# Optimization experiments

Measured on AMD Instinct MI355X. Metric: run time of the kernel, lower is better.

Reference implementation:

```python
import jax, jax.numpy as jnp
import numpy as np

EPS = 1e-09

def setup_inputs() -> dict:
    key = jax.random.key(0)
    k1, k2 = jax.random.split(key)
    N, D = 8192, 1024
    src_pos = jax.random.normal(k1, (N, D), dtype=jnp.float32)
    trg_pos = jax.random.normal(k2, (N, D), dtype=jnp.float32)
    return {"src_pos": src_pos, "trg_pos": trg_pos, "batch_size": N}

def reference(src_pos, trg_pos, batch_size):
    # [N, N] pairwise similarity (computed once; original redundantly does it twice)
    S = jnp.einsum('nd,md->nm', src_pos, trg_pos)
    S_xi_yi = jnp.diagonal(S)                      # [N] positive-pair scores
    lse = jax.nn.logsumexp(S, axis=1)              # [N] stable log-sum-exp over rows
    n = src_pos.shape[0]                           # matches torch assert fallback
    return -((S_xi_yi - lse).sum() / n) + EPS
```

## Files before the change

### kernel.cpp

```cpp
#include <hip/hip_runtime.h>
#include <hip/hip_bf16.h>
#include <math.h>

typedef __attribute__((ext_vector_type(4))) int   i32x4;
typedef __attribute__((ext_vector_type(4))) float f32x4;

#define NTOT 8192
#define DIM  1024
#define NCHUNK 128
#define QSCALE 20.0f
#define INV_S2 (1.0f / (QSCALE * QSCALE))

__device__ __forceinline__ void gload_lds16(const void* g, void* l) {
  __builtin_amdgcn_global_load_lds(
      (const __attribute__((address_space(1))) unsigned int*)g,
      (__attribute__((address_space(3))) unsigned int*)l,
      16, 0, 0);
}

#define SBAR() do { __builtin_amdgcn_sched_barrier(0); __builtin_amdgcn_s_barrier(); } while (0)

#define MFMA_PH(MQ, NQ, A, B)                                                        \
  do {                                                                               \
    __builtin_amdgcn_s_setprio(1);                                                   \
    _Pragma("unroll")                                                                \
    for (int fm = 0; fm < 4; ++fm) {                                                 \
      _Pragma("unroll")                                                              \
      for (int fn = 0; fn < 2; ++fn) {                                               \
        acc[(MQ)*4+fm][(NQ)*2+fn] = __builtin_amdgcn_mfma_i32_16x16x64_i8(           \
            A[fm][0], B[fn][0], acc[(MQ)*4+fm][(NQ)*2+fn], 0, 0, 0);                 \
        acc[(MQ)*4+fm][(NQ)*2+fn] = __builtin_amdgcn_mfma_i32_16x16x64_i8(           \
            A[fm][1], B[fn][1], acc[(MQ)*4+fm][(NQ)*2+fn], 0, 0, 0);                 \
      }                                                                              \
    }                                                                                \
    __builtin_amdgcn_s_setprio(0);                                                   \
  } while (0)

__global__ __launch_bounds__(256)
void convert_diag(const float* __restrict__ src, const float* __restrict__ trg,
                  unsigned int* __restrict__ A8, unsigned int* __restrict__ B8,
                  float* __restrict__ diag) {
  const int row  = blockIdx.x * 4 + (threadIdx.x >> 6);
  const int lane = threadIdx.x & 63;
  const f32x4* a = (const f32x4*)(src + (size_t)row * DIM);
  const f32x4* b = (const f32x4*)(trg + (size_t)row * DIM);
  float s = 0.f;
#pragma unroll
  for (int j = 0; j < 4; ++j) {
    f32x4 x = a[j * 64 + lane];
    f32x4 y = b[j * 64 + lane];
    s += x.x * y.x + x.y * y.y + x.z * y.z + x.w * y.w;
    unsigned pa = 0, pb = 0;
#pragma unroll
    for (int e = 0; e < 4; ++e) {
      float xf = (e == 0) ? x.x : (e == 1) ? x.y : (e == 2) ? x.z : x.w;
      float yf = (e == 0) ? y.x : (e == 1) ? y.y : (e == 2) ? y.z : y.w;
      int qa = (int)rintf(fminf(fmaxf(xf * QSCALE, -127.f), 127.f));
      int qb = (int)rintf(fminf(fmaxf(yf * QSCALE, -127.f), 127.f));
      pa |= ((unsigned)qa & 0xFFu) << (8 * e);
      pb |= ((unsigned)qb & 0xFFu) << (8 * e);
    }
    A8[(size_t)row * 256 + j * 64 + lane] = pa;
    B8[(size_t)row * 256 + j * 64 + lane] = pb;
  }
#pragma unroll
  for (int off = 32; off; off >>= 1) s += __shfl_xor(s, off);
  if (lane == 0) diag[row] = s;
}

__global__ __launch_bounds__(512, 2)
void gemm_lse(const unsigned char* __restrict__ A8, const unsigned char* __restrict__ B8,
              float2* __restrict__ partials) {
  __shared__ __align__(16) char lds[131072];
  char* As = lds;
  char* Bs = lds + 65536;

  const int tid  = threadIdx.x;
  const int lane = tid & 63;
  const int wid  = tid >> 6;
  const int wr = wid >> 2, wc = wid & 3;
  const int bx = blockIdx.x, by = blockIdx.y;
  const int row0 = by * 256, col0 = bx * 256;

  const int lrow = tid >> 3;
  const int lchk = tid & 7;
  const int schk = lchk ^ (lrow & 7);

  auto stageA = [&](int b, int h, int t) {
#pragma unroll
    for (int hi = 0; hi < 2; ++hi) {
      char* dst = As + (((b * 2 + h) * 2 + hi) << 13) + lrow * 128 + lchk * 16;
      const unsigned char* srcp = A8 + (size_t)(row0 + hi * 128 + h * 64 + lrow) * DIM
                                     + t * 128 + schk * 16;
      gload_lds16(srcp, dst);
    }
  };
  auto stageB = [&](int b, int h, int t) {
#pragma unroll
    for (int j = 0; j < 2; ++j) {
      char* dst = Bs + ((b * 2 + h) << 14) + j * 8192 + lrow * 128 + lchk * 16;
      const unsigned char* srcp = B8 + (size_t)(col0 + (2 * j + (lrow >> 5)) * 64 + h * 32 + (lrow & 31)) * DIM
                                     + t * 128 + schk * 16;
      gload_lds16(srcp, dst);
    }
  };

  const int arow = (lane & 15) * 128;
  const int kb0 = (((lane >> 4) * 16)     ) ^ ((lane & 7) << 4);
  const int kb1 = (((lane >> 4) * 16) + 64) ^ ((lane & 7) << 4);

  auto rdA = [&](i32x4 (&a)[4][2], int b, int h) {
    const char* base = As + (((b * 2 + h) * 2 + wr) << 13);
#pragma unroll
    for (int f = 0; f < 4; ++f) {
      a[f][0] = *(const i32x4*)(base + f * 2048 + arow + kb0);
      a[f][1] = *(const i32x4*)(base + f * 2048 + arow + kb1);
    }
  };
  auto rdB = [&](i32x4 (&bb)[2][2], int b, int h) {
    const char* base = Bs + ((b * 2 + h) << 14) + wc * 4096;
#pragma unroll
    for (int f = 0; f < 2; ++f) {
      bb[f][0] = *(const i32x4*)(base + f * 2048 + arow + kb0);
      bb[f][1] = *(const i32x4*)(base + f * 2048 + arow + kb1);
    }
  };

  i32x4 acc[8][4] = {};
  i32x4 a_lo[4][2], a_hi[4][2], b_lo[2][2], b_hi[2][2];

  stageA(0, 0, 0); stageA(0, 1, 0); stageB(0, 0, 0); stageB(0, 1, 0);
  stageA(1, 0, 1); stageB(1, 0, 1); stageB(1, 1, 1);
  asm volatile("s_waitcnt vmcnt(6)" ::: "memory");
  SBAR();

  for (int i = 0; i < 4; ++i) {
    const bool last = (i == 3);
    const int t1 = 2 * i + 1, t2 = 2 * i + 2, t3 = 2 * i + 3;

    rdA(a_lo, 0, 0); rdB(b_lo, 0, 0);
    stageA(1, 1, t1);
    SBAR();
    MFMA_PH(0, 0, a_lo, b_lo);
    SBAR();

    rdB(b_hi, 0, 1);
    if (!last) stageA(0, 0, t2);
    SBAR();
    MFMA_PH(0, 1, a_lo, b_hi);
    SBAR();

    rdA(a_hi, 0, 1);
    if (!last) stageB(0, 0, t2);
    SBAR();
    MFMA_PH(1, 1, a_hi, b_hi);
    SBAR();

    if (!last) stageB(0, 1, t2);
    SBAR();
    MFMA_PH(1, 0, a_hi, b_lo);
    if (last) { asm volatile("s_waitcnt vmcnt(0)" ::: "memory"); }
    else      { asm volatile("s_waitcnt vmcnt(6)" ::: "memory"); }
    SBAR();

    rdA(a_lo, 1, 0); rdB(b_lo, 1, 0);
    if (!last) stageA(0, 1, t2);
    SBAR();
    MFMA_PH(0, 0, a_lo, b_lo);
    SBAR();

    rdB(b_hi, 1, 1);
    if (!last) stageA(1, 0, t3);
    SBAR();
    MFMA_PH(0, 1, a_lo, b_hi);
    SBAR();

    rdA(a_hi, 1, 1);
    if (!last) stageB(1, 0, t3);
    SBAR();
    MFMA_PH(1, 1, a_hi, b_hi);
    SBAR();

    if (!last) stageB(1, 1, t3);
    SBAR();
    MFMA_PH(1, 0, a_hi, b_lo);
    if (!last) { asm volatile("s_waitcnt vmcnt(6)" ::: "memory"); }
    SBAR();
  }

  const int rbase  = row0 + wr * 128 + ((lane >> 4) << 2);
  const int cchunk = bx * 4 + wc;
#pragma unroll
  for (int mi = 0; mi < 8; ++mi) {
#pragma unroll
    for (int j = 0; j < 4; ++j) {
      int im = max(max(acc[mi][0][j], acc[mi][1][j]),
                   max(acc[mi][2][j], acc[mi][3][j]));
#pragma unroll
      for (int off = 8; off; off >>= 1) im = max(im, __shfl_xor(im, off));
      float l = 0.f;
#pragma unroll
      for (int ni = 0; ni < 4; ++ni)
        l += __expf((float)(acc[mi][ni][j] - im) * INV_S2);
#pragma unroll
      for (int off = 8; off; off >>= 1) l += __shfl_xor(l, off);
      if ((lane & 15) == 0)
        partials[(size_t)(rbase + mi * 16 + j) * NCHUNK + cchunk] =
            make_float2((float)im * INV_S2, l);
    }
  }
}

__global__ __launch_bounds__(256)
void row_lse_kernel(const float2* __restrict__ partials,
                    const float* __restrict__ diag,
                    float* __restrict__ rowval) {
  const int row  = (blockIdx.x * 256 + threadIdx.x) >> 6;
  const int lane = threadIdx.x & 63;
  if (row >= NTOT) return;
  const float2 p0 = partials[(size_t)row * NCHUNK + lane];
  const float2 p1 = partials[(size_t)row * NCHUNK + 64 + lane];
  float m = fmaxf(p0.x, p1.x);
#pragma unroll
  for (int off = 32; off; off >>= 1) m = fmaxf(m, __shfl_xor(m, off));
  float l = p0.y * __expf(p0.x - m) + p1.y * __expf(p1.x - m);
#pragma unroll
  for (int off = 32; off; off >>= 1) l += __shfl_xor(l, off);
  if (lane == 0) rowval[row] = diag[row] - (m + __logf(l));
}

__global__ __launch_bounds__(256)
void final_reduce(const float* __restrict__ rowval, float* __restrict__ out) {
  __shared__ float sm[4];
  float s = 0.f;
  for (int i = threadIdx.x; i < NTOT; i += 256) s += rowval[i];
#pragma unroll
  for (int off = 32; off; off >>= 1) s += __shfl_xor(s, off);
  if ((threadIdx.x & 63) == 0) sm[threadIdx.x >> 6] = s;
  __syncthreads();
  if (threadIdx.x == 0) {
    float t = sm[0] + sm[1] + sm[2] + sm[3];
    out[0] = -(t / (float)NTOT) + 1e-9f;
  }
}

extern "C" void kernel_launch(void* const* d_in, const int* in_sizes, int n_in,
                              void* d_out, int out_size, void* d_ws, size_t ws_size,
                              hipStream_t stream) {
  const float* src = (const float*)d_in[0];
  const float* trg = (const float*)d_in[1];
  float* out = (float*)d_out;

  unsigned char* A8 = (unsigned char*)d_ws;
  unsigned char* B8 = A8 + (size_t)NTOT * DIM;
  float2* partials = (float2*)((char*)d_ws + (size_t)16 * 1024 * 1024);
  float*  diag     = (float*)((char*)d_ws + (size_t)24 * 1024 * 1024);
  float*  rowval   = diag + NTOT;

  convert_diag<<<NTOT / 4, 256, 0, stream>>>(src, trg,
      (unsigned int*)A8, (unsigned int*)B8, diag);

  dim3 grid(NTOT / 256, NTOT / 256);
  gemm_lse<<<grid, 512, 0, stream>>>(A8, B8, partials);

  row_lse_kernel<<<NTOT / 4, 256, 0, stream>>>(partials, diag, rowval);
  final_reduce<<<1, 256, 0, stream>>>(rowval, out);
}
```

Measured before the change: 127.2 us.

## Drop pre-MFMA barriers in GEMM loop and fuse final reduction via atomics

Removes the workgroup barrier between each LDS-read/stage-issue step and the following MFMA phase in the int8 GEMM main loop, keeping only the barrier after each MFMA phase, so waves can start matrix math without waiting for the whole block. Separately, the final_reduce kernel is folded into row_lse_kernel: each block atomically adds its partial sum, and the last block (found with an atomic counter) writes the output. The accumulator and counter are zeroed in the convert kernel. This saves one kernel launch and some barrier stalls. The cost is a risk of LDS hazards if the removed barriers were needed, plus a non-deterministic float summation order.

```diff
diff --git a/kernel.cpp b/kernel.cpp
--- a/kernel.cpp
+++ b/kernel.cpp
@@ -39,7 +39,9 @@
 __global__ __launch_bounds__(256)
 void convert_diag(const float* __restrict__ src, const float* __restrict__ trg,
                   unsigned int* __restrict__ A8, unsigned int* __restrict__ B8,
-                  float* __restrict__ diag) {
+                  float* __restrict__ diag, float* __restrict__ rowsum,
+                  unsigned int* __restrict__ ctr) {
+  if (blockIdx.x == 0 && threadIdx.x == 0) { *rowsum = 0.f; *ctr = 0u; }
   const int row  = blockIdx.x * 4 + (threadIdx.x >> 6);
   const int lane = threadIdx.x & 63;
   const f32x4* a = (const f32x4*)(src + (size_t)row * DIM);
@@ -140,24 +142,17 @@
 
     rdA(a_lo, 0, 0); rdB(b_lo, 0, 0);
     stageA(1, 1, t1);
-    SBAR();
     MFMA_PH(0, 0, a_lo, b_lo);
     SBAR();
-
     rdB(b_hi, 0, 1);
     if (!last) stageA(0, 0, t2);
-    SBAR();
     MFMA_PH(0, 1, a_lo, b_hi);
     SBAR();
-
     rdA(a_hi, 0, 1);
     if (!last) stageB(0, 0, t2);
-    SBAR();
     MFMA_PH(1, 1, a_hi, b_hi);
     SBAR();
-
     if (!last) stageB(0, 1, t2);
-    SBAR();
     MFMA_PH(1, 0, a_hi, b_lo);
     if (last) { asm volatile("s_waitcnt vmcnt(0)" ::: "memory"); }
     else      { asm volatile("s_waitcnt vmcnt(6)" ::: "memory"); }
@@ -165,24 +160,17 @@
 
     rdA(a_lo, 1, 0); rdB(b_lo, 1, 0);
     if (!last) stageA(0, 1, t2);
-    SBAR();
     MFMA_PH(0, 0, a_lo, b_lo);
     SBAR();
-
     rdB(b_hi, 1, 1);
     if (!last) stageA(1, 0, t3);
-    SBAR();
     MFMA_PH(0, 1, a_lo, b_hi);
     SBAR();
-
     rdA(a_hi, 1, 1);
     if (!last) stageB(1, 0, t3);
-    SBAR();
     MFMA_PH(1, 1, a_hi, b_hi);
     SBAR();
-
     if (!last) stageB(1, 1, t3);
-    SBAR();
     MFMA_PH(1, 0, a_hi, b_lo);
     if (!last) { asm volatile("s_waitcnt vmcnt(6)" ::: "memory"); }
     SBAR();
@@ -214,10 +202,10 @@
 __global__ __launch_bounds__(256)
 void row_lse_kernel(const float2* __restrict__ partials,
                     const float* __restrict__ diag,
-                    float* __restrict__ rowval) {
+                    float* __restrict__ rowsum, unsigned int* __restrict__ ctr,
+                    float* __restrict__ out) {
   const int row  = (blockIdx.x * 256 + threadIdx.x) >> 6;
   const int lane = threadIdx.x & 63;
-  if (row >= NTOT) return;
   const float2 p0 = partials[(size_t)row * NCHUNK + lane];
   const float2 p1 = partials[(size_t)row * NCHUNK + 64 + lane];
   float m = fmaxf(p0.x, p1.x);
@@ -226,20 +214,19 @@
   float l = p0.y * __expf(p0.x - m) + p1.y * __expf(p1.x - m);
 #pragma unroll
   for (int off = 32; off; off >>= 1) l += __shfl_xor(l, off);
-  if (lane == 0) rowval[row] = diag[row] - (m + __logf(l));
-}
-
-__global__ __launch_bounds__(256)
-void final_reduce(const float* __restrict__ rowval, float* __restrict__ out) {
+
   __shared__ float sm[4];
-  float s = 0.f;
-  for (int i = threadIdx.x; i < NTOT; i += 256) s += rowval[i];
-#pragma unroll
-  for (int off = 32; off; off >>= 1) s += __shfl_xor(s, off);
-  if ((threadIdx.x & 63) == 0) sm[threadIdx.x >> 6] = s;
+  __shared__ bool last_blk;
+  if (lane == 0) sm[threadIdx.x >> 6] = diag[row] - (m + __logf(l));
   __syncthreads();
   if (threadIdx.x == 0) {
-    float t = sm[0] + sm[1] + sm[2] + sm[3];
+    atomicAdd(rowsum, sm[0] + sm[1] + sm[2] + sm[3]);
+    __threadfence();
+    last_blk = (atomicAdd(ctr, 1u) == (unsigned)(NTOT / 4 - 1));
+  }
+  __syncthreads();
+  if (threadIdx.x == 0 && last_blk) {
+    float t = atomicAdd(rowsum, 0.0f);
     out[0] = -(t / (float)NTOT) + 1e-9f;
   }
 }
@@ -255,14 +242,14 @@
   unsigned char* B8 = A8 + (size_t)NTOT * DIM;
   float2* partials = (float2*)((char*)d_ws + (size_t)16 * 1024 * 1024);
   float*  diag     = (float*)((char*)d_ws + (size_t)24 * 1024 * 1024);
-  float*  rowval   = diag + NTOT;
+  float*  rowsum   = diag + NTOT;
+  unsigned int* ctr = (unsigned int*)(rowsum + 1);
 
   convert_diag<<<NTOT / 4, 256, 0, stream>>>(src, trg,
-      (unsigned int*)A8, (unsigned int*)B8, diag);
+      (unsigned int*)A8, (unsigned int*)B8, diag, rowsum, ctr);
 
   dim3 grid(NTOT / 256, NTOT / 256);
   gemm_lse<<<grid, 512, 0, stream>>>(A8, B8, partials);
 
-  row_lse_kernel<<<NTOT / 4, 256, 0, stream>>>(partials, diag, rowval);
-  final_reduce<<<1, 256, 0, stream>>>(rowval, out);
-}
+  row_lse_kernel<<<NTOT / 4, 256, 0, stream>>>(partials, diag, rowsum, ctr, out);
+}
```

Measured after the change: 167.9 us. +32.0%, slower.

## Switch to 32x32x32 int8 MFMA with pre-tiled operand layout from convert kernel

Applied to the files above, without the earlier changes.

The conversion kernel now writes the int8 operands in a tiled, MFMA-fragment-ordered layout, so the GEMM stages contiguous 16-byte chunks per thread and reads fragments linearly from LDS without swizzle math. The GEMM moves from 16x16x64 to 32x32x32 int8 MFMA with 16-wide accumulators, and drops the barrier between LDS reads and each MFMA phase. The epilogue row reductions are adjusted to the 32x32 output layout. Removing those barriers risks LDS read/write races between stages, and the new write pattern in the convert kernel may coalesce less well.

```diff
diff --git a/kernel.cpp b/kernel.cpp
--- a/kernel.cpp
+++ b/kernel.cpp
@@ -2,8 +2,9 @@
 #include <hip/hip_bf16.h>
 #include <math.h>
 
-typedef __attribute__((ext_vector_type(4))) int   i32x4;
-typedef __attribute__((ext_vector_type(4))) float f32x4;
+typedef __attribute__((ext_vector_type(4)))  int   i32x4;
+typedef __attribute__((ext_vector_type(16))) int   i32x16;
+typedef __attribute__((ext_vector_type(4)))  float f32x4;
 
 #define NTOT 8192
 #define DIM  1024
@@ -24,13 +25,11 @@
   do {                                                                               \
     __builtin_amdgcn_s_setprio(1);                                                   \
     _Pragma("unroll")                                                                \
-    for (int fm = 0; fm < 4; ++fm) {                                                 \
+    for (int fm = 0; fm < 2; ++fm) {                                                 \
       _Pragma("unroll")                                                              \
-      for (int fn = 0; fn < 2; ++fn) {                                               \
-        acc[(MQ)*4+fm][(NQ)*2+fn] = __builtin_amdgcn_mfma_i32_16x16x64_i8(           \
-            A[fm][0], B[fn][0], acc[(MQ)*4+fm][(NQ)*2+fn], 0, 0, 0);                 \
-        acc[(MQ)*4+fm][(NQ)*2+fn] = __builtin_amdgcn_mfma_i32_16x16x64_i8(           \
-            A[fm][1], B[fn][1], acc[(MQ)*4+fm][(NQ)*2+fn], 0, 0, 0);                 \
+      for (int k = 0; k < 4; ++k) {                                                  \
+        acc[(MQ)*2+fm][(NQ)] = __builtin_amdgcn_mfma_i32_32x32x32_i8(                \
+            A[fm][k], B[k], acc[(MQ)*2+fm][(NQ)], 0, 0, 0);                          \
       }                                                                              \
     }                                                                                \
     __builtin_amdgcn_s_setprio(0);                                                   \
@@ -38,15 +37,25 @@
 
 __global__ __launch_bounds__(256)
 void convert_diag(const float* __restrict__ src, const float* __restrict__ trg,
-                  unsigned int* __restrict__ A8, unsigned int* __restrict__ B8,
+                  unsigned char* __restrict__ A8, unsigned char* __restrict__ B8,
                   float* __restrict__ diag) {
   const int row  = blockIdx.x * 4 + (threadIdx.x >> 6);
   const int lane = threadIdx.x & 63;
+  const int rr = row & 255, bt = row >> 8;
+  const size_t aRow = (size_t)bt * 262144 + (size_t)((rr >> 6) & 1) * 16384
+                    + (size_t)(rr >> 7) * 8192 + (size_t)((rr >> 5) & 1) * 4096
+                    + (size_t)(rr & 31) * 16;
+  const size_t bRow = (size_t)bt * 262144 + (size_t)((rr >> 5) & 1) * 16384
+                    + (size_t)(rr >> 7) * 8192 + (size_t)((rr >> 6) & 1) * 4096
+                    + (size_t)(rr & 31) * 16;
   const f32x4* a = (const f32x4*)(src + (size_t)row * DIM);
   const f32x4* b = (const f32x4*)(trg + (size_t)row * DIM);
   float s = 0.f;
 #pragma unroll
   for (int j = 0; j < 4; ++j) {
+    const int k0 = j * 256 + lane * 4;
+    const size_t kPart = (size_t)(k0 >> 7) * 32768 + (size_t)((k0 >> 5) & 3) * 1024
+                       + (size_t)((k0 >> 4) & 1) * 512 + (size_t)(k0 & 15);
     f32x4 x = a[j * 64 + lane];
     f32x4 y = b[j * 64 + lane];
     s += x.x * y.x + x.y * y.y + x.z * y.z + x.w * y.w;
@@ -60,8 +69,8 @@
       pa |= ((unsigned)qa & 0xFFu) << (8 * e);
       pb |= ((unsigned)qb & 0xFFu) << (8 * e);
     }
-    A8[(size_t)row * 256 + j * 64 + lane] = pa;
-    B8[(size_t)row * 256 + j * 64 + lane] = pb;
+    *(unsigned int*)(A8 + aRow + kPart) = pa;
+    *(unsigned int*)(B8 + bRow + kPart) = pb;
   }
 #pragma unroll
   for (int off = 32; off; off >>= 1) s += __shfl_xor(s, off);
@@ -80,54 +89,42 @@
   const int wid  = tid >> 6;
   const int wr = wid >> 2, wc = wid & 3;
   const int bx = blockIdx.x, by = blockIdx.y;
-  const int row0 = by * 256, col0 = bx * 256;
-
-  const int lrow = tid >> 3;
-  const int lchk = tid & 7;
-  const int schk = lchk ^ (lrow & 7);
+  const int row0 = by * 256;
+
+  const unsigned char* Abase = A8 + (size_t)by * 262144;
+  const unsigned char* Bbase = B8 + (size_t)bx * 262144;
 
   auto stageA = [&](int b, int h, int t) {
 #pragma unroll
-    for (int hi = 0; hi < 2; ++hi) {
-      char* dst = As + (((b * 2 + h) * 2 + hi) << 13) + lrow * 128 + lchk * 16;
-      const unsigned char* srcp = A8 + (size_t)(row0 + hi * 128 + h * 64 + lrow) * DIM
-                                     + t * 128 + schk * 16;
-      gload_lds16(srcp, dst);
-    }
+    for (int sub = 0; sub < 2; ++sub)
+      gload_lds16(Abase + (size_t)t * 32768 + h * 16384 + sub * 8192 + tid * 16,
+                  As + (b * 2 + h) * 16384 + sub * 8192 + tid * 16);
   };
   auto stageB = [&](int b, int h, int t) {
 #pragma unroll
-    for (int j = 0; j < 2; ++j) {
-      char* dst = Bs + ((b * 2 + h) << 14) + j * 8192 + lrow * 128 + lchk * 16;
-      const unsigned char* srcp = B8 + (size_t)(col0 + (2 * j + (lrow >> 5)) * 64 + h * 32 + (lrow & 31)) * DIM
-                                     + t * 128 + schk * 16;
-      gload_lds16(srcp, dst);
-    }
-  };
-
-  const int arow = (lane & 15) * 128;
-  const int kb0 = (((lane >> 4) * 16)     ) ^ ((lane & 7) << 4);
-  const int kb1 = (((lane >> 4) * 16) + 64) ^ ((lane & 7) << 4);
-
-  auto rdA = [&](i32x4 (&a)[4][2], int b, int h) {
-    const char* base = As + (((b * 2 + h) * 2 + wr) << 13);
-#pragma unroll
-    for (int f = 0; f < 4; ++f) {
-      a[f][0] = *(const i32x4*)(base + f * 2048 + arow + kb0);
-      a[f][1] = *(const i32x4*)(base + f * 2048 + arow + kb1);
-    }
-  };
-  auto rdB = [&](i32x4 (&bb)[2][2], int b, int h) {
-    const char* base = Bs + ((b * 2 + h) << 14) + wc * 4096;
-#pragma unroll
-    for (int f = 0; f < 2; ++f) {
-      bb[f][0] = *(const i32x4*)(base + f * 2048 + arow + kb0);
-      bb[f][1] = *(const i32x4*)(base + f * 2048 + arow + kb1);
-    }
-  };
-
-  i32x4 acc[8][4] = {};
-  i32x4 a_lo[4][2], a_hi[4][2], b_lo[2][2], b_hi[2][2];
+    for (int sub = 0; sub < 2; ++sub)
+      gload_lds16(Bbase + (size_t)t * 32768 + h * 16384 + sub * 8192 + tid * 16,
+                  Bs + (b * 2 + h) * 16384 + sub * 8192 + tid * 16);
+  };
+
+  auto rdA = [&](i32x4 (&a)[2][4], int b, int MQ) {
+    const char* base = As + (b * 2 + MQ) * 16384 + wr * 8192 + lane * 16;
+#pragma unroll
+    for (int f = 0; f < 2; ++f)
+#pragma unroll
+      for (int k = 0; k < 4; ++k)
+        a[f][k] = *(const i32x4*)(base + (f * 4 + k) * 1024);
+  };
+  auto rdB = [&](i32x4 (&bb)[4], int b, int NQ) {
+    const char* base = Bs + (b * 2 + NQ) * 16384 + (wc >> 1) * 8192 + (wc & 1) * 4096
+                     + lane * 16;
+#pragma unroll
+    for (int k = 0; k < 4; ++k)
+      bb[k] = *(const i32x4*)(base + k * 1024);
+  };
+
+  i32x16 acc[4][2] = {};
+  i32x4 a_lo[2][4], a_hi[2][4], b_lo[4], b_hi[4];
 
   stageA(0, 0, 0); stageA(0, 1, 0); stageB(0, 0, 0); stageB(0, 1, 0);
   stageA(1, 0, 1); stageB(1, 0, 1); stageB(1, 1, 1);
@@ -140,24 +137,17 @@
 
     rdA(a_lo, 0, 0); rdB(b_lo, 0, 0);
     stageA(1, 1, t1);
-    SBAR();
     MFMA_PH(0, 0, a_lo, b_lo);
     SBAR();
-
     rdB(b_hi, 0, 1);
     if (!last) stageA(0, 0, t2);
-    SBAR();
     MFMA_PH(0, 1, a_lo, b_hi);
     SBAR();
-
     rdA(a_hi, 0, 1);
     if (!last) stageB(0, 0, t2);
-    SBAR();
     MFMA_PH(1, 1, a_hi, b_hi);
     SBAR();
-
     if (!last) stageB(0, 1, t2);
-    SBAR();
     MFMA_PH(1, 0, a_hi, b_lo);
     if (last) { asm volatile("s_waitcnt vmcnt(0)" ::: "memory"); }
     else      { asm volatile("s_waitcnt vmcnt(6)" ::: "memory"); }
@@ -165,48 +155,45 @@
 
     rdA(a_lo, 1, 0); rdB(b_lo, 1, 0);
     if (!last) stageA(0, 1, t2);
-    SBAR();
     MFMA_PH(0, 0, a_lo, b_lo);
     SBAR();
-
     rdB(b_hi, 1, 1);
     if (!last) stageA(1, 0, t3);
-    SBAR();
     MFMA_PH(0, 1, a_lo, b_hi);
     SBAR();
-
     rdA(a_hi, 1, 1);
     if (!last) stageB(1, 0, t3);
-    SBAR();
     MFMA_PH(1, 1, a_hi, b_hi);
     SBAR();
-
     if (!last) stageB(1, 1, t3);
-    SBAR();
     MFMA_PH(1, 0, a_hi, b_lo);
     if (!last) { asm volatile("s_waitcnt vmcnt(6)" ::: "memory"); }
     SBAR();
   }
 
-  const int rbase  = row0 + wr * 128 + ((lane >> 4) << 2);
+  const int hi = lane >> 5;
+  const int rbase = row0 + wr * 128 + 4 * hi;
   const int cchunk = bx * 4 + wc;
 #pragma unroll
-  for (int mi = 0; mi < 8; ++mi) {
-#pragma unroll
-    for (int j = 0; j < 4; ++j) {
-      int im = max(max(acc[mi][0][j], acc[mi][1][j]),
-                   max(acc[mi][2][j], acc[mi][3][j]));
-#pragma unroll
-      for (int off = 8; off; off >>= 1) im = max(im, __shfl_xor(im, off));
-      float l = 0.f;
-#pragma unroll
-      for (int ni = 0; ni < 4; ++ni)
-        l += __expf((float)(acc[mi][ni][j] - im) * INV_S2);
-#pragma unroll
-      for (int off = 8; off; off >>= 1) l += __shfl_xor(l, off);
-      if ((lane & 15) == 0)
-        partials[(size_t)(rbase + mi * 16 + j) * NCHUNK + cchunk] =
-            make_float2((float)im * INV_S2, l);
+  for (int mi = 0; mi < 4; ++mi) {
+#pragma unroll
+    for (int q = 0; q < 4; ++q) {
+#pragma unroll
+      for (int j = 0; j < 4; ++j) {
+        const int r = q * 4 + j;
+        int v0 = acc[mi][0][r];
+        int v1 = acc[mi][1][r];
+        int im = max(v0, v1);
+#pragma unroll
+        for (int off = 16; off; off >>= 1) im = max(im, __shfl_xor(im, off));
+        float l = __expf((float)(v0 - im) * INV_S2) + __expf((float)(v1 - im) * INV_S2);
+#pragma unroll
+        for (int off = 16; off; off >>= 1) l += __shfl_xor(l, off);
+        if ((lane & 31) == 0) {
+          const int row = rbase + mi * 32 + 8 * q + j;
+          partials[(size_t)row * NCHUNK + cchunk] = make_float2((float)im * INV_S2, l);
+        }
+      }
     }
   }
 }
@@ -257,8 +244,7 @@
   float*  diag     = (float*)((char*)d_ws + (size_t)24 * 1024 * 1024);
   float*  rowval   = diag + NTOT;
 
-  convert_diag<<<NTOT / 4, 256, 0, stream>>>(src, trg,
-      (unsigned int*)A8, (unsigned int*)B8, diag);
+  convert_diag<<<NTOT / 4, 256, 0, stream>>>(src, trg, A8, B8, diag);
 
   dim3 grid(NTOT / 256, NTOT / 256);
   gemm_lse<<<grid, 512, 0, stream>>>(A8, B8, partials);
```

After: 183.3 us. 44.1% more time.

## Shrink int8 GEMM block tile to 128x128 with 256 threads, drop intra-phase barriers

Applied to the files above, without the earlier changes.

Reduces the fused GEMM+LSE block tile from 256x256 (8 waves) to 128x128 (4 waves), halving LDS use to 64KB and giving each wave a 64x64 sub-tile. Staging and fragment-read addressing, the accumulator arrays and the epilogue indexing are rewritten to match, and the grid grows fourfold. It also removes the barrier between each LDS read/stage-issue and its MFMA phase, keeping only the barrier after each phase. The goal is more resident blocks and fewer barrier stalls, at the cost of lower per-block data reuse, more global/L2 traffic and a possible LDS race with fewer barriers.

```diff
diff --git a/kernel.cpp b/kernel.cpp
--- a/kernel.cpp
+++ b/kernel.cpp
@@ -24,13 +24,13 @@
   do {                                                                               \
     __builtin_amdgcn_s_setprio(1);                                                   \
     _Pragma("unroll")                                                                \
-    for (int fm = 0; fm < 4; ++fm) {                                                 \
+    for (int fm = 0; fm < 2; ++fm) {                                                 \
       _Pragma("unroll")                                                              \
       for (int fn = 0; fn < 2; ++fn) {                                               \
-        acc[(MQ)*4+fm][(NQ)*2+fn] = __builtin_amdgcn_mfma_i32_16x16x64_i8(           \
-            A[fm][0], B[fn][0], acc[(MQ)*4+fm][(NQ)*2+fn], 0, 0, 0);                 \
-        acc[(MQ)*4+fm][(NQ)*2+fn] = __builtin_amdgcn_mfma_i32_16x16x64_i8(           \
-            A[fm][1], B[fn][1], acc[(MQ)*4+fm][(NQ)*2+fn], 0, 0, 0);                 \
+        acc[(MQ)*2+fm][(NQ)*2+fn] = __builtin_amdgcn_mfma_i32_16x16x64_i8(           \
+            A[fm][0], B[fn][0], acc[(MQ)*2+fm][(NQ)*2+fn], 0, 0, 0);                 \
+        acc[(MQ)*2+fm][(NQ)*2+fn] = __builtin_amdgcn_mfma_i32_16x16x64_i8(           \
+            A[fm][1], B[fn][1], acc[(MQ)*2+fm][(NQ)*2+fn], 0, 0, 0);                 \
       }                                                                              \
     }                                                                                \
     __builtin_amdgcn_s_setprio(0);                                                   \
@@ -68,19 +68,19 @@
   if (lane == 0) diag[row] = s;
 }
 
-__global__ __launch_bounds__(512, 2)
+__global__ __launch_bounds__(256, 2)
 void gemm_lse(const unsigned char* __restrict__ A8, const unsigned char* __restrict__ B8,
               float2* __restrict__ partials) {
-  __shared__ __align__(16) char lds[131072];
+  __shared__ __align__(16) char lds[65536];
   char* As = lds;
-  char* Bs = lds + 65536;
+  char* Bs = lds + 32768;
 
   const int tid  = threadIdx.x;
   const int lane = tid & 63;
   const int wid  = tid >> 6;
-  const int wr = wid >> 2, wc = wid & 3;
+  const int wr = wid >> 1, wc = wid & 1;
   const int bx = blockIdx.x, by = blockIdx.y;
-  const int row0 = by * 256, col0 = bx * 256;
+  const int row0 = by * 128, col0 = bx * 128;
 
   const int lrow = tid >> 3;
   const int lchk = tid & 7;
@@ -89,45 +89,45 @@
   auto stageA = [&](int b, int h, int t) {
 #pragma unroll
     for (int hi = 0; hi < 2; ++hi) {
-      char* dst = As + (((b * 2 + h) * 2 + hi) << 13) + lrow * 128 + lchk * 16;
-      const unsigned char* srcp = A8 + (size_t)(row0 + hi * 128 + h * 64 + lrow) * DIM
+      char* dst = As + (((b * 2 + h) * 2 + hi) << 12) + lrow * 128 + lchk * 16;
+      const unsigned char* srcp = A8 + (size_t)(row0 + hi * 64 + h * 32 + lrow) * DIM
                                      + t * 128 + schk * 16;
       gload_lds16(srcp, dst);
     }
   };
   auto stageB = [&](int b, int h, int t) {
 #pragma unroll
-    for (int j = 0; j < 2; ++j) {
-      char* dst = Bs + ((b * 2 + h) << 14) + j * 8192 + lrow * 128 + lchk * 16;
-      const unsigned char* srcp = B8 + (size_t)(col0 + (2 * j + (lrow >> 5)) * 64 + h * 32 + (lrow & 31)) * DIM
+    for (int hi = 0; hi < 2; ++hi) {
+      char* dst = Bs + (((b * 2 + h) * 2 + hi) << 12) + lrow * 128 + lchk * 16;
+      const unsigned char* srcp = B8 + (size_t)(col0 + hi * 64 + h * 32 + lrow) * DIM
                                      + t * 128 + schk * 16;
       gload_lds16(srcp, dst);
     }
   };
 
-  const int arow = (lane & 15) * 128;
+  const int arow0 = (lane & 15) * 128;
   const int kb0 = (((lane >> 4) * 16)     ) ^ ((lane & 7) << 4);
   const int kb1 = (((lane >> 4) * 16) + 64) ^ ((lane & 7) << 4);
 
-  auto rdA = [&](i32x4 (&a)[4][2], int b, int h) {
-    const char* base = As + (((b * 2 + h) * 2 + wr) << 13);
-#pragma unroll
-    for (int f = 0; f < 4; ++f) {
-      a[f][0] = *(const i32x4*)(base + f * 2048 + arow + kb0);
-      a[f][1] = *(const i32x4*)(base + f * 2048 + arow + kb1);
-    }
-  };
-  auto rdB = [&](i32x4 (&bb)[2][2], int b, int h) {
-    const char* base = Bs + ((b * 2 + h) << 14) + wc * 4096;
+  auto rdA = [&](i32x4 (&a)[2][2], int b, int MQ) {
+    const char* base = As + (((b * 2 + MQ) * 2 + wr) << 12);
 #pragma unroll
     for (int f = 0; f < 2; ++f) {
-      bb[f][0] = *(const i32x4*)(base + f * 2048 + arow + kb0);
-      bb[f][1] = *(const i32x4*)(base + f * 2048 + arow + kb1);
-    }
-  };
-
-  i32x4 acc[8][4] = {};
-  i32x4 a_lo[4][2], a_hi[4][2], b_lo[2][2], b_hi[2][2];
+      a[f][0] = *(const i32x4*)(base + f * 2048 + arow0 + kb0);
+      a[f][1] = *(const i32x4*)(base + f * 2048 + arow0 + kb1);
+    }
+  };
+  auto rdB = [&](i32x4 (&bb)[2][2], int b, int NQ) {
+    const char* base = Bs + (((b * 2 + NQ) * 2 + wc) << 12);
+#pragma unroll
+    for (int f = 0; f < 2; ++f) {
+      bb[f][0] = *(const i32x4*)(base + f * 2048 + arow0 + kb0);
+      bb[f][1] = *(const i32x4*)(base + f * 2048 + arow0 + kb1);
+    }
+  };
+
+  i32x4 acc[4][4] = {};
+  i32x4 a_lo[2][2], a_hi[2][2], b_lo[2][2], b_hi[2][2];
 
   stageA(0, 0, 0); stageA(0, 1, 0); stageB(0, 0, 0); stageB(0, 1, 0);
   stageA(1, 0, 1); stageB(1, 0, 1); stageB(1, 1, 1);
@@ -140,24 +140,17 @@
 
     rdA(a_lo, 0, 0); rdB(b_lo, 0, 0);
     stageA(1, 1, t1);
-    SBAR();
     MFMA_PH(0, 0, a_lo, b_lo);
     SBAR();
-
     rdB(b_hi, 0, 1);
     if (!last) stageA(0, 0, t2);
-    SBAR();
     MFMA_PH(0, 1, a_lo, b_hi);
     SBAR();
-
     rdA(a_hi, 0, 1);
     if (!last) stageB(0, 0, t2);
-    SBAR();
     MFMA_PH(1, 1, a_hi, b_hi);
     SBAR();
-
     if (!last) stageB(0, 1, t2);
-    SBAR();
     MFMA_PH(1, 0, a_hi, b_lo);
     if (last) { asm volatile("s_waitcnt vmcnt(0)" ::: "memory"); }
     else      { asm volatile("s_waitcnt vmcnt(6)" ::: "memory"); }
@@ -165,33 +158,26 @@
 
     rdA(a_lo, 1, 0); rdB(b_lo, 1, 0);
     if (!last) stageA(0, 1, t2);
-    SBAR();
     MFMA_PH(0, 0, a_lo, b_lo);
     SBAR();
-
     rdB(b_hi, 1, 1);
     if (!last) stageA(1, 0, t3);
-    SBAR();
     MFMA_PH(0, 1, a_lo, b_hi);
     SBAR();
-
     rdA(a_hi, 1, 1);
     if (!last) stageB(1, 0, t3);
-    SBAR();
     MFMA_PH(1, 1, a_hi, b_hi);
     SBAR();
-
     if (!last) stageB(1, 1, t3);
-    SBAR();
     MFMA_PH(1, 0, a_hi, b_lo);
     if (!last) { asm volatile("s_waitcnt vmcnt(6)" ::: "memory"); }
     SBAR();
   }
 
-  const int rbase  = row0 + wr * 128 + ((lane >> 4) << 2);
-  const int cchunk = bx * 4 + wc;
-#pragma unroll
-  for (int mi = 0; mi < 8; ++mi) {
+  const int rbase  = row0 + wr * 64 + ((lane >> 4) << 2);
+  const int cchunk = bx * 2 + wc;
+#pragma unroll
+  for (int mi = 0; mi < 4; ++mi) {
 #pragma unroll
     for (int j = 0; j < 4; ++j) {
       int im = max(max(acc[mi][0][j], acc[mi][1][j]),
@@ -260,8 +246,8 @@
   convert_diag<<<NTOT / 4, 256, 0, stream>>>(src, trg,
       (unsigned int*)A8, (unsigned int*)B8, diag);
 
-  dim3 grid(NTOT / 256, NTOT / 256);
-  gemm_lse<<<grid, 512, 0, stream>>>(A8, B8, partials);
+  dim3 grid(NTOT / 128, NTOT / 128);
+  gemm_lse<<<grid, 256, 0, stream>>>(A8, B8, partials);
 
   row_lse_kernel<<<NTOT / 4, 256, 0, stream>>>(partials, diag, rowval);
   final_reduce<<<1, 256, 0, stream>>>(rowval, out);
```

After: 143.1 us. 1.13x slower.
